# Optimization experiments

Measured on AMD Instinct MI355X. Metric: run time of the kernel, lower is better.

The kernel has to match this reference:

```python
import jax, jax.numpy as jnp
import numpy as np

# R-FCN PSRoI pooling constants (match init_kwargs)
P = 7          # pooled_height == pooled_width
GS = 7         # group_size
D = 21         # output_dim
SCALE = 0.0625 # spatial_scale (1/16)


def setup_inputs() -> dict:
    key = jax.random.key(0)
    k1, k2, k3, k4 = jax.random.split(key, 4)
    N, C, H, W = 4, D * GS * GS, 80, 80   # C = output_dim * group_size^2
    R = 2048
    features = jax.random.normal(k1, (N, C, H, W), dtype=jnp.float32)
    img = H / SCALE  # 1280 px image
    bidx = jax.random.randint(k2, (R,), 0, N).astype(jnp.float32)
    xy1 = jax.random.uniform(k3, (R, 2), minval=0.0, maxval=img * 0.6)
    wh = jax.random.uniform(k4, (R, 2), minval=img * 0.05, maxval=img * 0.4)
    xy2 = jnp.clip(xy1 + wh, 0.0, img - 1.0)
    rois = jnp.concatenate([bidx[:, None], xy1, xy2], axis=1)  # [R,5]: (b,x1,y1,x2,y2)
    return {"features": features, "rois": rois}


def reference(features, rois):
    """Position-sensitive RoI pooling (R-FCN psroi_pooling_forward_cuda semantics).

    Each output bin (ctop, ph, pw) averages feature channel
    c = (ctop*GS + gh)*GS + gw over the bin's integer pixel region.
    Bin sums are computed exactly via a 2D integral image, turning the
    irregular per-bin reduction into 4 gathers per bin.
    """
    N, C, H, W = features.shape
    R = rois.shape[0]

    # Integral image: ii[n,c,i,j] = sum of features[n,c,:i,:j]; shape [N,C,H+1,W+1]
    ii = jnp.pad(
        jnp.cumsum(jnp.cumsum(features, axis=2), axis=3),
        ((0, 0), (0, 0), (1, 0), (1, 0)),
    )

    b = rois[:, 0].astype(jnp.int32)                       # [R]
    x1 = jnp.round(rois[:, 1]) * SCALE
    y1 = jnp.round(rois[:, 2]) * SCALE
    x2 = (jnp.round(rois[:, 3]) + 1.0) * SCALE
    y2 = (jnp.round(rois[:, 4]) + 1.0) * SCALE
    bin_w = jnp.maximum(x2 - x1, 0.1) / P                  # [R]
    bin_h = jnp.maximum(y2 - y1, 0.1) / P

    g = jnp.arange(P, dtype=jnp.float32)                   # bin index grid
    hs = jnp.clip(jnp.floor(g[None, :] * bin_h[:, None] + y1[:, None]), 0, H).astype(jnp.int32)        # [R,P]
    he = jnp.clip(jnp.ceil((g[None, :] + 1.0) * bin_h[:, None] + y1[:, None]), 0, H).astype(jnp.int32)
    ws = jnp.clip(jnp.floor(g[None, :] * bin_w[:, None] + x1[:, None]), 0, W).astype(jnp.int32)
    we = jnp.clip(jnp.ceil((g[None, :] + 1.0) * bin_w[:, None] + x1[:, None]), 0, W).astype(jnp.int32)

    # Position-sensitive channel map: c[ctop,ph,pw] = (ctop*GS+gh)*GS+gw
    ctop = jnp.arange(D)[:, None, None]
    gh = jnp.clip((jnp.arange(P) * GS) // P, 0, GS - 1)[None, :, None]
    gw = jnp.clip((jnp.arange(P) * GS) // P, 0, GS - 1)[None, None, :]
    cmap = (ctop * GS + gh) * GS + gw                      # [D,P,P]

    # Broadcast gather indices to [R,D,P,P]
    B = b[:, None, None, None]
    Cc = cmap[None]
    HS = hs[:, None, :, None]; HE = he[:, None, :, None]
    WS = ws[:, None, None, :]; WE = we[:, None, None, :]

    s = ii[B, Cc, HE, WE] - ii[B, Cc, HS, WE] - ii[B, Cc, HE, WS] + ii[B, Cc, HS, WS]
    area = ((HE - HS) * (WE - WS)).astype(features.dtype)
    out = jnp.where(area > 0, s / jnp.maximum(area, 1.0), jnp.zeros((), features.dtype))
    return out  # [R, D, P, P]
```

## Files before the change

kernel.cpp:

```cpp
#include <hip/hip_runtime.h>

#define P   7
#define GS  7
#define D   21
#define HH  80
#define WW  80
#define CC  (D * GS * GS)
#define PLANE (HH * WW)
#define IW  84
#define NSEG 5
#define SEGLEN 16

__device__ __forceinline__ float recip7() {
    union { unsigned u; float f; } c; c.u = 0x3E124925u; return c.f;
}

__device__ __forceinline__ float mul_add_nofma(float a, float b, float c) {
    float t = a * b;
    asm volatile("" : "+v"(t));
    return t + c;
}

__device__ __forceinline__ void edges_for(const float* __restrict__ roi,
                                          int gh, int gw,
                                          unsigned& hp, unsigned& wp)
{
    float x1 = rintf(roi[1]) * 0.0625f;
    float y1 = rintf(roi[2]) * 0.0625f;
    float x2 = (rintf(roi[3]) + 1.0f) * 0.0625f;
    float y2 = (rintf(roi[4]) + 1.0f) * 0.0625f;
    float bin_w = fmaxf(x2 - x1, 0.1f) * recip7();
    float bin_h = fmaxf(y2 - y1, 0.1f) * recip7();
    asm volatile("" : "+v"(bin_w), "+v"(bin_h));
    int hs = (int)fminf(fmaxf(floorf(mul_add_nofma((float)gh,       bin_h, y1)), 0.0f), 80.0f);
    int he = (int)fminf(fmaxf(ceilf (mul_add_nofma((float)(gh + 1), bin_h, y1)), 0.0f), 80.0f);
    int ws = (int)fminf(fmaxf(floorf(mul_add_nofma((float)gw,       bin_w, x1)), 0.0f), 80.0f);
    int we = (int)fminf(fmaxf(ceilf (mul_add_nofma((float)(gw + 1), bin_w, x1)), 0.0f), 80.0f);
    hp = (unsigned)(hs | (he << 8));
    wp = (unsigned)(ws | (we << 8));
}

__global__ __launch_bounds__(1024) void prep_kernel(
    const float* __restrict__ rois, int R, int N,
    int* __restrict__ jlist, int* __restrict__ base)
{
    __shared__ unsigned char bsh[2048];
    __shared__ int wcnt[16][8];
    __shared__ int wbase[16][8];
    __shared__ int baseS[9];
    int tid = threadIdx.x, wave = tid >> 6, lane = tid & 63;

    for (int r = tid; r < R; r += 1024)
        bsh[r] = (unsigned char)(int)rois[(size_t)r * 5];
    __syncthreads();

    int chunk = (R + 15) / 16;
    int rbeg = wave * chunk;
    int rend = min(rbeg + chunk, R);
    int cnt[8];
    #pragma unroll
    for (int b = 0; b < 8; ++b) cnt[b] = 0;
    for (int rr = rbeg + lane; rr < rend; rr += 64) {
        int bv = bsh[rr];
        #pragma unroll
        for (int b = 0; b < 8; ++b) {
            if (b < N) cnt[b] += __popcll(__ballot(bv == b));
        }
    }
    if (lane == 0) {
        #pragma unroll
        for (int b = 0; b < 8; ++b) wcnt[wave][b] = cnt[b];
    }
    __syncthreads();

    if (tid < 8) {
        int b = tid, acc = 0;
        for (int w = 0; w < 16; ++w) { wbase[w][b] = acc; acc += wcnt[w][b]; }
        baseS[b] = acc;
    }
    __syncthreads();
    if (tid == 0) {
        int acc = 0;
        for (int b = 0; b < N; ++b) { int t = baseS[b]; baseS[b] = acc; acc += t; }
        baseS[N] = acc;
    }
    __syncthreads();

    {
        int off[8];
        #pragma unroll
        for (int b = 0; b < 8; ++b) off[b] = (b < N) ? (baseS[b] + wbase[wave][b]) : 0;
        for (int rr = rbeg + lane; rr < rend; rr += 64) {
            int bv = bsh[rr];
            #pragma unroll
            for (int b = 0; b < 8; ++b) {
                if (b < N) {
                    unsigned long long mask = __ballot(bv == b);
                    if (bv == b) {
                        int pos = off[b] + __popcll(mask & ((1ull << lane) - 1ull));
                        jlist[pos] = rr;
                    }
                    off[b] += __popcll(mask);
                }
            }
        }
    }
    if (tid <= N) base[tid] = baseS[tid];
}

__global__ __launch_bounds__(512) void psroi_plane_kernel(
    const float* __restrict__ feat, const float* __restrict__ rois, int R,
    const int* __restrict__ jlist, const int* __restrict__ base,
    float* __restrict__ dst)
{
    __shared__ float ii[HH * IW];
    __shared__ float tot[NSEG][HH];

    int tid = threadIdx.x;
    int bid = blockIdx.x;
    int b   = bid / CC;
    int c   = bid % CC;
    int rem = c % (GS * GS);
    int gh  = rem / GS;
    int gw  = rem % GS;

    const float4* src4 = (const float4*)(feat + ((size_t)b * CC + c) * PLANE);
    for (int i = tid; i < PLANE / 4; i += 512) {
        float4 v = src4[i];
        int h = i / 20;
        int w = (i % 20) * 4;
        *(float4*)(&ii[h * IW + w]) = v;
    }

    int j0 = base[b], j1 = base[b + 1];
    int jA = j0 + tid, jB = jA + 512, jC = jA + 1024, jD = jA + 1536;
    unsigned hA = 0, wA = 0, hB = 0, wB = 0, hC = 0, wC = 0, hD = 0, wD = 0;
    if (jA < j1) edges_for(rois + (size_t)jlist[jA] * 5, gh, gw, hA, wA);
    if (jB < j1) edges_for(rois + (size_t)jlist[jB] * 5, gh, gw, hB, wB);
    if (jC < j1) edges_for(rois + (size_t)jlist[jC] * 5, gh, gw, hC, wC);
    if (jD < j1) edges_for(rois + (size_t)jlist[jD] * 5, gh, gw, hD, wD);

    __syncthreads();

    bool act = tid < NSEG * WW;
    int seg = tid / WW;
    int lw  = tid % WW;

    {
        float v[SEGLEN];
        int col = lw, h0 = seg * SEGLEN;
        if (act) {
            float s = 0.0f;
            #pragma unroll
            for (int k = 0; k < SEGLEN; ++k) { v[k] = ii[(h0 + k) * IW + col]; s += v[k]; }
            tot[seg][lw] = s;
        }
        __syncthreads();
        if (act) {
            float off = 0.0f;
            #pragma unroll
            for (int jj = 0; jj < NSEG - 1; ++jj) if (jj < seg) off += tot[jj][lw];
            float run = off;
            #pragma unroll
            for (int k = 0; k < SEGLEN; ++k) { run += v[k]; ii[(h0 + k) * IW + col] = run; }
        }
        __syncthreads();
    }
    {
        float4 q0, q1, q2, q3;
        int row = lw, w0 = seg * SEGLEN;
        float4* rp = (float4*)&ii[row * IW + w0];
        if (act) {
            q0 = rp[0]; q1 = rp[1]; q2 = rp[2]; q3 = rp[3];
            float s;
            s  = q0.x; s += q0.y; s += q0.z; s += q0.w;
            s += q1.x; s += q1.y; s += q1.z; s += q1.w;
            s += q2.x; s += q2.y; s += q2.z; s += q2.w;
            s += q3.x; s += q3.y; s += q3.z; s += q3.w;
            tot[seg][row] = s;
        }
        __syncthreads();
        if (act) {
            float off = 0.0f;
            #pragma unroll
            for (int jj = 0; jj < NSEG - 1; ++jj) if (jj < seg) off += tot[jj][row];
            float run = off;
            run += q0.x; q0.x = run; run += q0.y; q0.y = run;
            run += q0.z; q0.z = run; run += q0.w; q0.w = run;
            run += q1.x; q1.x = run; run += q1.y; q1.y = run;
            run += q1.z; q1.z = run; run += q1.w; q1.w = run;
            run += q2.x; q2.x = run; run += q2.y; q2.y = run;
            run += q2.z; q2.z = run; run += q2.w; q2.w = run;
            run += q3.x; q3.x = run; run += q3.y; q3.y = run;
            run += q3.z; q3.z = run; run += q3.w; q3.w = run;
            rp[0] = q0; rp[1] = q1; rp[2] = q2; rp[3] = q3;
        }
        __syncthreads();
    }

    #define IIV(hq, wq) ( ((hq) > 0 && (wq) > 0)                              \
        ? ii[((hq) - 1) * IW + ((wq) - 1)] : 0.0f )
    #define EMIT(jX, hX, wX)                                                  \
    if (jX < j1) {                                                            \
        int hs = hX & 255, he = (int)(hX >> 8);                               \
        int ws = wX & 255, we = (int)(wX >> 8);                               \
        float s = ((IIV(he, we) - IIV(hs, we))                                \
                 -  IIV(he, ws)) + IIV(hs, ws);                               \
        int area = (he - hs) * (we - ws);                                     \
        dst[(size_t)c * R + jX] = (area > 0) ? (s / (float)area) : 0.0f;      \
    }
    EMIT(jA, hA, wA)
    EMIT(jB, hB, wB)
    EMIT(jC, hC, wC)
    EMIT(jD, hD, wD)
    #undef EMIT
    #undef IIV
}

__global__ __launch_bounds__(256) void transpose_kernel(
    const float* __restrict__ in, const int* __restrict__ jlist,
    float* __restrict__ out, int R, int C)
{
    __shared__ float t[64][65];
    __shared__ int rows[64];
    int j0 = blockIdx.x * 64;
    int c0 = blockIdx.y * 64;
    int tx = threadIdx.x, ty = threadIdx.y;
    int tid = ty * 64 + tx;

    if (tid < 64 && j0 + tid < R) rows[tid] = jlist[j0 + tid];

    #pragma unroll
    for (int k0 = 0; k0 < 64; k0 += 4) {
        int k = k0 + ty;
        int cc = c0 + k, jj = j0 + tx;
        if (cc < C && jj < R) t[k][tx] = in[(size_t)cc * R + jj];
    }
    __syncthreads();
    #pragma unroll
    for (int k0 = 0; k0 < 64; k0 += 4) {
        int k = k0 + ty;
        int cc = c0 + tx;
        if (j0 + k < R && cc < C) out[(size_t)rows[k] * C + cc] = t[tx][k];
    }
}

__global__ __launch_bounds__(256) void psroi_fallback_kernel(
    const float* __restrict__ feat, const float* __restrict__ rois,
    int R, float* __restrict__ out)
{
    __shared__ float ii[81 * 81];
    int bid = blockIdx.x;
    int b = bid / CC, c = bid % CC;
    int rem = c % 49, gh = rem / 7, gw = rem % 7;

    const float* plane = feat + ((size_t)b * CC + c) * PLANE;
    for (int i = threadIdx.x; i < PLANE; i += 256) {
        int h = i / WW, w = i % WW;
        ii[(h + 1) * 81 + (w + 1)] = plane[i];
    }
    for (int i = threadIdx.x; i < 81; i += 256) { ii[i] = 0.0f; ii[i * 81] = 0.0f; }
    __syncthreads();
    if (threadIdx.x < WW) {
        int w = threadIdx.x + 1; float s = 0.0f;
        for (int h = 1; h <= HH; ++h) { s += ii[h * 81 + w]; ii[h * 81 + w] = s; }
    }
    __syncthreads();
    if (threadIdx.x < HH) {
        int h = threadIdx.x + 1; float* row = &ii[h * 81]; float s = 0.0f;
        for (int w = 1; w <= WW; ++w) { s += row[w]; row[w] = s; }
    }
    __syncthreads();
    for (int r = threadIdx.x; r < R; r += 256) {
        const float* roi = rois + (size_t)r * 5;
        if ((int)roi[0] != b) continue;
        unsigned hp, wp;
        edges_for(roi, gh, gw, hp, wp);
        int hs = hp & 255, he = (int)(hp >> 8);
        int ws = wp & 255, we = (int)(wp >> 8);
        float s = ii[he * 81 + we] - ii[hs * 81 + we] - ii[he * 81 + ws] + ii[hs * 81 + ws];
        int area = (he - hs) * (we - ws);
        out[(size_t)r * CC + c] = (area > 0) ? (s / (float)area) : 0.0f;
    }
}

extern "C" void kernel_launch(void* const* d_in, const int* in_sizes, int n_in,
                              void* d_out, int out_size, void* d_ws, size_t ws_size,
                              hipStream_t stream)
{
    const float* feat = (const float*)d_in[0];
    const float* rois = (const float*)d_in[1];
    float* out        = (float*)d_out;

    int R = in_sizes[1] / 5;
    int N = in_sizes[0] / (CC * PLANE);

    size_t off_wsT  = 0;
    size_t off_jl   = (off_wsT + (size_t)CC * R * sizeof(float) + 15) & ~(size_t)15;
    size_t off_base = off_jl + (size_t)R * sizeof(int);
    size_t need     = off_base + (size_t)(N + 1) * sizeof(int);

    bool chunk_ok = (((R + 15) / 16) % 64) == 0;

    if (ws_size >= need && N <= 8 && R <= 2048 && chunk_ok) {
        char* ws = (char*)d_ws;
        float* ws_T = (float*)(ws + off_wsT);
        int*   jl   = (int*)(ws + off_jl);
        int*   base = (int*)(ws + off_base);

        prep_kernel<<<1, 1024, 0, stream>>>(rois, R, N, jl, base);
        psroi_plane_kernel<<<N * CC, 512, 0, stream>>>(feat, rois, R, jl, base, ws_T);
        dim3 blk(64, 4), grd((R + 63) / 64, (CC + 63) / 64);
        transpose_kernel<<<grd, blk, 0, stream>>>(ws_T, jl, out, R, CC);
    } else {
        psroi_fallback_kernel<<<N * CC, 256, 0, stream>>>(feat, rois, R, out);
    }
}
```

Before: 43.60 us.

## Drop RoI bucketing prep kernel; filter RoIs by batch index per block

Removes the single-block prep kernel that sorted RoIs by batch index into a compacted list. Each plane block now scans all R RoIs, reads each batch index, and only emits results for RoIs matching its batch. Scatter in the transpose becomes a direct row-order write. This eliminates one serial kernel launch and an indirection, but each thread now does masked work with more divergence and more RoI reads per block.

```diff
diff --git a/kernel.cpp b/kernel.cpp
--- a/kernel.cpp
+++ b/kernel.cpp
@@ -40,77 +40,8 @@
     wp = (unsigned)(ws | (we << 8));
 }
 
-__global__ __launch_bounds__(1024) void prep_kernel(
-    const float* __restrict__ rois, int R, int N,
-    int* __restrict__ jlist, int* __restrict__ base)
-{
-    __shared__ unsigned char bsh[2048];
-    __shared__ int wcnt[16][8];
-    __shared__ int wbase[16][8];
-    __shared__ int baseS[9];
-    int tid = threadIdx.x, wave = tid >> 6, lane = tid & 63;
-
-    for (int r = tid; r < R; r += 1024)
-        bsh[r] = (unsigned char)(int)rois[(size_t)r * 5];
-    __syncthreads();
-
-    int chunk = (R + 15) / 16;
-    int rbeg = wave * chunk;
-    int rend = min(rbeg + chunk, R);
-    int cnt[8];
-    #pragma unroll
-    for (int b = 0; b < 8; ++b) cnt[b] = 0;
-    for (int rr = rbeg + lane; rr < rend; rr += 64) {
-        int bv = bsh[rr];
-        #pragma unroll
-        for (int b = 0; b < 8; ++b) {
-            if (b < N) cnt[b] += __popcll(__ballot(bv == b));
-        }
-    }
-    if (lane == 0) {
-        #pragma unroll
-        for (int b = 0; b < 8; ++b) wcnt[wave][b] = cnt[b];
-    }
-    __syncthreads();
-
-    if (tid < 8) {
-        int b = tid, acc = 0;
-        for (int w = 0; w < 16; ++w) { wbase[w][b] = acc; acc += wcnt[w][b]; }
-        baseS[b] = acc;
-    }
-    __syncthreads();
-    if (tid == 0) {
-        int acc = 0;
-        for (int b = 0; b < N; ++b) { int t = baseS[b]; baseS[b] = acc; acc += t; }
-        baseS[N] = acc;
-    }
-    __syncthreads();
-
-    {
-        int off[8];
-        #pragma unroll
-        for (int b = 0; b < 8; ++b) off[b] = (b < N) ? (baseS[b] + wbase[wave][b]) : 0;
-        for (int rr = rbeg + lane; rr < rend; rr += 64) {
-            int bv = bsh[rr];
-            #pragma unroll
-            for (int b = 0; b < 8; ++b) {
-                if (b < N) {
-                    unsigned long long mask = __ballot(bv == b);
-                    if (bv == b) {
-                        int pos = off[b] + __popcll(mask & ((1ull << lane) - 1ull));
-                        jlist[pos] = rr;
-                    }
-                    off[b] += __popcll(mask);
-                }
-            }
-        }
-    }
-    if (tid <= N) base[tid] = baseS[tid];
-}
-
 __global__ __launch_bounds__(512) void psroi_plane_kernel(
     const float* __restrict__ feat, const float* __restrict__ rois, int R,
-    const int* __restrict__ jlist, const int* __restrict__ base,
     float* __restrict__ dst)
 {
     __shared__ float ii[HH * IW];
@@ -132,13 +63,16 @@
         *(float4*)(&ii[h * IW + w]) = v;
     }
 
-    int j0 = base[b], j1 = base[b + 1];
-    int jA = j0 + tid, jB = jA + 512, jC = jA + 1024, jD = jA + 1536;
+    int rA = tid, rB = tid + 512, rC = tid + 1024, rD = tid + 1536;
+    bool mA = (rA < R) && ((int)rois[(size_t)rA * 5] == b);
+    bool mB = (rB < R) && ((int)rois[(size_t)rB * 5] == b);
+    bool mC = (rC < R) && ((int)rois[(size_t)rC * 5] == b);
+    bool mD = (rD < R) && ((int)rois[(size_t)rD * 5] == b);
     unsigned hA = 0, wA = 0, hB = 0, wB = 0, hC = 0, wC = 0, hD = 0, wD = 0;
-    if (jA < j1) edges_for(rois + (size_t)jlist[jA] * 5, gh, gw, hA, wA);
-    if (jB < j1) edges_for(rois + (size_t)jlist[jB] * 5, gh, gw, hB, wB);
-    if (jC < j1) edges_for(rois + (size_t)jlist[jC] * 5, gh, gw, hC, wC);
-    if (jD < j1) edges_for(rois + (size_t)jlist[jD] * 5, gh, gw, hD, wD);
+    if (mA) edges_for(rois + (size_t)rA * 5, gh, gw, hA, wA);
+    if (mB) edges_for(rois + (size_t)rB * 5, gh, gw, hB, wB);
+    if (mC) edges_for(rois + (size_t)rC * 5, gh, gw, hC, wC);
+    if (mD) edges_for(rois + (size_t)rD * 5, gh, gw, hD, wD);
 
     __syncthreads();
 
@@ -200,48 +134,43 @@
 
     #define IIV(hq, wq) ( ((hq) > 0 && (wq) > 0)                              \
         ? ii[((hq) - 1) * IW + ((wq) - 1)] : 0.0f )
-    #define EMIT(jX, hX, wX)                                                  \
-    if (jX < j1) {                                                            \
+    #define EMIT(mX, rX, hX, wX)                                              \
+    if (mX) {                                                                 \
         int hs = hX & 255, he = (int)(hX >> 8);                               \
         int ws = wX & 255, we = (int)(wX >> 8);                               \
         float s = ((IIV(he, we) - IIV(hs, we))                                \
                  -  IIV(he, ws)) + IIV(hs, ws);                               \
         int area = (he - hs) * (we - ws);                                     \
-        dst[(size_t)c * R + jX] = (area > 0) ? (s / (float)area) : 0.0f;      \
-    }
-    EMIT(jA, hA, wA)
-    EMIT(jB, hB, wB)
-    EMIT(jC, hC, wC)
-    EMIT(jD, hD, wD)
+        dst[(size_t)c * R + rX] = (area > 0) ? (s / (float)area) : 0.0f;      \
+    }
+    EMIT(mA, rA, hA, wA)
+    EMIT(mB, rB, hB, wB)
+    EMIT(mC, rC, hC, wC)
+    EMIT(mD, rD, hD, wD)
     #undef EMIT
     #undef IIV
 }
 
 __global__ __launch_bounds__(256) void transpose_kernel(
-    const float* __restrict__ in, const int* __restrict__ jlist,
-    float* __restrict__ out, int R, int C)
+    const float* __restrict__ in, float* __restrict__ out, int R, int C)
 {
     __shared__ float t[64][65];
-    __shared__ int rows[64];
-    int j0 = blockIdx.x * 64;
+    int r0 = blockIdx.x * 64;
     int c0 = blockIdx.y * 64;
     int tx = threadIdx.x, ty = threadIdx.y;
-    int tid = ty * 64 + tx;
-
-    if (tid < 64 && j0 + tid < R) rows[tid] = jlist[j0 + tid];
 
     #pragma unroll
     for (int k0 = 0; k0 < 64; k0 += 4) {
         int k = k0 + ty;
-        int cc = c0 + k, jj = j0 + tx;
-        if (cc < C && jj < R) t[k][tx] = in[(size_t)cc * R + jj];
+        int cc = c0 + k, rr = r0 + tx;
+        if (cc < C && rr < R) t[k][tx] = in[(size_t)cc * R + rr];
     }
     __syncthreads();
     #pragma unroll
     for (int k0 = 0; k0 < 64; k0 += 4) {
         int k = k0 + ty;
-        int cc = c0 + tx;
-        if (j0 + k < R && cc < C) out[(size_t)rows[k] * C + cc] = t[tx][k];
+        int rr = r0 + k, cc = c0 + tx;
+        if (rr < R && cc < C) out[(size_t)rr * C + cc] = t[tx][k];
     }
 }
 
@@ -295,23 +224,13 @@
     int R = in_sizes[1] / 5;
     int N = in_sizes[0] / (CC * PLANE);
 
-    size_t off_wsT  = 0;
-    size_t off_jl   = (off_wsT + (size_t)CC * R * sizeof(float) + 15) & ~(size_t)15;
-    size_t off_base = off_jl + (size_t)R * sizeof(int);
-    size_t need     = off_base + (size_t)(N + 1) * sizeof(int);
-
-    bool chunk_ok = (((R + 15) / 16) % 64) == 0;
-
-    if (ws_size >= need && N <= 8 && R <= 2048 && chunk_ok) {
-        char* ws = (char*)d_ws;
-        float* ws_T = (float*)(ws + off_wsT);
-        int*   jl   = (int*)(ws + off_jl);
-        int*   base = (int*)(ws + off_base);
-
-        prep_kernel<<<1, 1024, 0, stream>>>(rois, R, N, jl, base);
-        psroi_plane_kernel<<<N * CC, 512, 0, stream>>>(feat, rois, R, jl, base, ws_T);
+    size_t need = (size_t)CC * R * sizeof(float);
+
+    if (ws_size >= need && N <= 8 && R <= 2048) {
+        float* ws_T = (float*)d_ws;
+        psroi_plane_kernel<<<N * CC, 512, 0, stream>>>(feat, rois, R, ws_T);
         dim3 blk(64, 4), grd((R + 63) / 64, (CC + 63) / 64);
-        transpose_kernel<<<grd, blk, 0, stream>>>(ws_T, jl, out, R, CC);
+        transpose_kernel<<<grd, blk, 0, stream>>>(ws_T, out, R, CC);
     } else {
         psroi_fallback_kernel<<<N * CC, 256, 0, stream>>>(feat, rois, R, out);
     }
```

Measured after the change: 50.75 us. +16.4%, slower.
